# Kernel optimization log

Hardware: AMD Instinct MI355X
Metric: run time of the kernel (lower is better)

The kernel has to match this reference:

```python
import jax, jax.numpy as jnp
import numpy as np

NEG = -1e9  # matches torch masked_fill value (additive, not -inf)

def setup_inputs() -> dict:
    key = jax.random.key(0)
    k1, k2, k3, k4 = jax.random.split(key, 4)
    B, H, S, D = 8, 16, 1024, 64
    q = jax.random.normal(k1, (B, H, S, D), dtype=jnp.float32)
    k = jax.random.normal(k2, (B, H, S, D), dtype=jnp.float32)
    v = jax.random.normal(k3, (B, H, S, D), dtype=jnp.float32)
    event_length = jax.random.randint(k4, (B,), 0, S, dtype=jnp.int32)
    return {"q": q, "k": k, "v": v, "event_length": event_length}

def reference(q, k, v, event_length):
    B, H, S, D = q.shape
    scale = 1.0 / jnp.sqrt(jnp.asarray(D, dtype=q.dtype))
    idx = jnp.arange(S)
    # valid[b, i] = i < event_length[b]
    valid = idx[None, :] < event_length[:, None]            # [B, S]
    # additive mask: 0 where (row valid AND col valid), else -1e9
    pair = valid[:, :, None] & valid[:, None, :]            # [B, S, S]
    attn_mask = jnp.where(pair, 0.0, NEG).astype(q.dtype)[:, None, :, :]  # [B,1,S,S]
    scores = jnp.einsum('bhqd,bhkd->bhqk', q, k) * scale + attn_mask
    probs = jax.nn.softmax(scores, axis=-1)
    out = jnp.einsum('bhqk,bhkd->bhqd', probs, v)
    return out
```

## Files before the change

### kernel.cpp

```cpp
#include <hip/hip_runtime.h>


#define Sdim 1024
#define Ddim 64
#define PITCH 72

typedef float f32x4 __attribute__((ext_vector_type(4)));
typedef _Float16 f16x8 __attribute__((ext_vector_type(8)));
typedef _Float16 f16x4 __attribute__((ext_vector_type(4)));
typedef unsigned short u16x8 __attribute__((ext_vector_type(8)));
typedef unsigned int u32x2 __attribute__((ext_vector_type(2)));

union FragU { u16x8 u; f16x8 h; };
union Frag4 { u32x2 u; f16x4 h; };

__device__ __forceinline__ unsigned pk2(float a, float b) {
  auto h = __builtin_amdgcn_cvt_pkrtz(a, b);
  return __builtin_bit_cast(unsigned, h);
}

__device__ __forceinline__ float fexp2(float x) {
  float r;
  asm("v_exp_f32 %0, %1" : "=v"(r) : "v"(x));
  return r;
}

__global__ __launch_bounds__(256, 3)
void attn_fwd(const float* __restrict__ Q, const float* __restrict__ K,
              const float* __restrict__ V, const int* __restrict__ EL,
              float* __restrict__ Out, unsigned* __restrict__ queues) {
  __shared__ unsigned short lds_all[2 * 64 * PITCH];
  __shared__ int s_item;
  unsigned short* k_lds = lds_all;
  unsigned short* v_lds = lds_all + 64 * PITCH;

  const int tid   = threadIdx.x;
  const int homeq = blockIdx.x & 7;
  unsigned* ctr = &queues[homeq * 32];

  const int w    = tid >> 6;
  const int lane = tid & 63;
  const int r    = lane & 15;
  const int hi   = lane >> 4;
  const int r3   = r >> 3;
  const int sr   = tid >> 4;
  const int sc   = tid & 15;
  const int vskew = ((sc >> 1) & 7) * 8;

  for (;;) {
    __syncthreads();
    if (tid == 0) s_item = (int)atomicAdd(ctr, 1u);
    __syncthreads();
    const int g = s_item;
    if (g >= 128) break;

    const int pan = g >> 3;
    const int qt  = g & 7;
    const int bh  = pan * 8 + homeq;
    const int L   = EL[bh >> 4];

    const size_t base = (size_t)bh * Sdim * Ddim;
    const float* Qb = Q + base;
    const float* Kb = K + base;
    const float* Vb = V + base;
    float* ob = Out + base;

    const int q0blk = qt * 128;

    if (q0blk >= L) {
      float* red = (float*)lds_all;
      const int sc4 = sc * 4;
      const float* vp = Vb + (size_t)sr * Ddim + sc4;
      float4 acc = {0.f, 0.f, 0.f, 0.f};
#pragma unroll 8
      for (int i = 0; i < 64; ++i) {
        float4 a = *(const float4*)(vp + (size_t)i * 16 * Ddim);
        acc.x += a.x; acc.y += a.y; acc.z += a.z; acc.w += a.w;
      }
      *(float4*)&red[sr * 68 + sc4] = acc;
      __syncthreads();
      if (tid < 16) {
        float4 s = {0.f, 0.f, 0.f, 0.f};
#pragma unroll
        for (int i = 0; i < 16; ++i) {
          float4 a = *(const float4*)&red[i * 68 + tid * 4];
          s.x += a.x; s.y += a.y; s.z += a.z; s.w += a.w;
        }
        const float inv = 1.0f / 1024.0f;
        s.x *= inv; s.y *= inv; s.z *= inv; s.w *= inv;
        *(float4*)&red[16 * 68 + tid * 4] = s;
      }
      __syncthreads();
      const float4 cm = *(const float4*)&red[16 * 68 + sc4];
#pragma unroll
      for (int pp = 0; pp < 8; ++pp) {
        int row = q0blk + pp * 16 + sr;
        *(float4*)&ob[(size_t)row * Ddim + sc4] = cm;
      }
      continue;
    }

    const int q0w      = q0blk + w * 32;
    const bool wValid  = q0w < L;
    const bool wAllVal = (q0w + 32) <= L;
    const int kFull    = (L + 63) >> 6;
    const int ktB      = L >> 6;
    const bool straddle = (q0blk + 128) > L;

    const bool qv0 = (q0w + r) < L;
    const bool qv1 = (q0w + 16 + r) < L;

    const float SCL = 0.125f * 1.44269504088896340736f;
    f16x8 qf[2][2];
    if (wValid) {
#pragma unroll
      for (int qc = 0; qc < 2; ++qc)
#pragma unroll
        for (int kk = 0; kk < 2; ++kk) {
          const float* pq = Qb + (size_t)(q0w + qc * 16 + r) * Ddim + kk * 32 + hi * 8;
          float4 a = *(const float4*)pq;
          float4 cc = *(const float4*)(pq + 4);
          union { unsigned u[4]; f16x8 hh; } f;
          f.u[0] = pk2(a.x * SCL, a.y * SCL);   f.u[1] = pk2(a.z * SCL, a.w * SCL);
          f.u[2] = pk2(cc.x * SCL, cc.y * SCL); f.u[3] = pk2(cc.z * SCL, cc.w * SCL);
          qf[qc][kk] = f.hh;
        }
    }

    const f32x4 zero4 = {0.f, 0.f, 0.f, 0.f};
    f32x4 otacc[2][4];
#pragma unroll
    for (int qc = 0; qc < 2; ++qc)
#pragma unroll
      for (int dc = 0; dc < 4; ++dc) otacc[qc][dc] = zero4;

    float lpart[2] = {0.f, 0.f};

    const float* pK = Kb + (size_t)sr * Ddim + sc * 4;
    const float* pV = Vb + (size_t)(sr * 4) * Ddim + sc * 4;

    float4 kpre[4], vpre[4];
    auto LOADK = [&](int k0_) {
#pragma unroll
      for (int i = 0; i < 4; ++i)
        kpre[i] = *(const float4*)(pK + (size_t)(k0_ + 16 * i) * Ddim);
    };
    auto LOADV = [&](int k0_) {
#pragma unroll
      for (int jj = 0; jj < 4; ++jj)
        vpre[jj] = *(const float4*)(pV + (size_t)(k0_ + jj) * Ddim);
    };

    LOADK(0);
    LOADV(0);

    for (int kt = 0; kt < kFull; ++kt) {
      const int k0 = kt * 64;
      __syncthreads();

#pragma unroll
      for (int i = 0; i < 4; ++i) {
        u32x2 o;
        o[0] = pk2(kpre[i].x, kpre[i].y); o[1] = pk2(kpre[i].z, kpre[i].w);
        *(u32x2*)&k_lds[(16 * i + sr) * PITCH + sc * 4] = o;
      }
      {
        const int cp = (sr * 4 + vskew) & 63;
        u32x2 o;
        o[0] = pk2(vpre[0].x, vpre[1].x); o[1] = pk2(vpre[2].x, vpre[3].x);
        *(u32x2*)&v_lds[(sc * 4 + 0) * PITCH + cp] = o;
        o[0] = pk2(vpre[0].y, vpre[1].y); o[1] = pk2(vpre[2].y, vpre[3].y);
        *(u32x2*)&v_lds[(sc * 4 + 1) * PITCH + cp] = o;
        o[0] = pk2(vpre[0].z, vpre[1].z); o[1] = pk2(vpre[2].z, vpre[3].z);
        *(u32x2*)&v_lds[(sc * 4 + 2) * PITCH + cp] = o;
        o[0] = pk2(vpre[0].w, vpre[1].w); o[1] = pk2(vpre[2].w, vpre[3].w);
        *(u32x2*)&v_lds[(sc * 4 + 3) * PITCH + cp] = o;
      }
      __syncthreads();

      if (kt + 1 < kFull) { LOADK(k0 + 64); LOADV(k0 + 64); }

      if (wValid) {
        f32x4 sacc[2][4];
#pragma unroll
        for (int qc = 0; qc < 2; ++qc)
#pragma unroll
          for (int kc = 0; kc < 4; ++kc) sacc[qc][kc] = zero4;

        __builtin_amdgcn_s_setprio(1);
#pragma unroll
        for (int kc = 0; kc < 4; ++kc)
#pragma unroll
          for (int kk = 0; kk < 2; ++kk) {
            FragU kf;
            kf.u = *(const u16x8*)&k_lds[(kc * 16 + r) * PITCH + kk * 32 + hi * 8];
            sacc[0][kc] = __builtin_amdgcn_mfma_f32_16x16x32_f16(kf.h, qf[0][kk], sacc[0][kc], 0, 0, 0);
            sacc[1][kc] = __builtin_amdgcn_mfma_f32_16x16x32_f16(kf.h, qf[1][kk], sacc[1][kc], 0, 0, 0);
          }
        __builtin_amdgcn_s_setprio(0);

        const bool noMask = wAllVal && (kt != ktB);
        Frag4 pf[2][4];
#pragma unroll
        for (int qc = 0; qc < 2; ++qc) {
          const bool qv = qc ? qv1 : qv0;
          float ls = 0.f;
#pragma unroll
          for (int kc = 0; kc < 4; ++kc) {
            float pr[4];
#pragma unroll
            for (int rg = 0; rg < 4; ++rg) {
              float s = sacc[qc][kc][rg];
              if (!noMask) {
                int kg = k0 + kc * 16 + 4 * hi + rg;
                s = (qv && kg < L) ? s : -__builtin_inff();
              }
              pr[rg] = fexp2(s);
              ls += pr[rg];
            }
            pf[qc][kc].u[0] = pk2(pr[0], pr[1]);
            pf[qc][kc].u[1] = pk2(pr[2], pr[3]);
          }
          lpart[qc] += ls;
        }

        __builtin_amdgcn_s_setprio(1);
#pragma unroll
        for (int kc = 0; kc < 4; ++kc)
#pragma unroll
          for (int dc = 0; dc < 4; ++dc) {
            const int col = (kc * 16 + 4 * hi + (((2 * dc + r3) & 7) << 3)) & 63;
            Frag4 vf;
            vf.u = *(const u32x2*)&v_lds[(dc * 16 + r) * PITCH + col];
            otacc[0][dc] = __builtin_amdgcn_mfma_f32_16x16x16f16(vf.h, pf[0][kc].h, otacc[0][dc], 0, 0, 0);
            otacc[1][dc] = __builtin_amdgcn_mfma_f32_16x16x16f16(vf.h, pf[1][kc].h, otacc[1][dc], 0, 0, 0);
          }
        __builtin_amdgcn_s_setprio(0);
      }
    }

    __syncthreads();
    float* scr = (float*)lds_all + w * (16 * 68);
#pragma unroll
    for (int qc = 0; qc < 2; ++qc) {
      float l = lpart[qc];
      l += __shfl_xor(l, 16, 64);
      l += __shfl_xor(l, 32, 64);
      const float inv = 1.0f / l;
      if (wValid) {
#pragma unroll
        for (int dc = 0; dc < 4; ++dc)
#pragma unroll
          for (int rg = 0; rg < 4; ++rg)
            scr[r * 68 + dc * 16 + 4 * hi + rg] = otacc[qc][dc][rg] * inv;
      }
      asm volatile("s_waitcnt lgkmcnt(0)" ::: "memory");
      __builtin_amdgcn_sched_barrier(0);
      if (wValid) {
        const int rowq = lane >> 2, cs = lane & 3;
        const int q = q0w + qc * 16 + rowq;
        if (q < L) {
#pragma unroll
          for (int i = 0; i < 4; ++i) {
            float4 vv = *(const float4*)&scr[rowq * 68 + cs * 16 + i * 4];
            *(float4*)&ob[(size_t)q * Ddim + cs * 16 + i * 4] = vv;
          }
        }
      }
      asm volatile("s_waitcnt lgkmcnt(0)" ::: "memory");
      __builtin_amdgcn_sched_barrier(0);
    }

    if (straddle) {
      __syncthreads();
      float* red = (float*)lds_all;
      const int sc4 = sc * 4;
      const float* vp = Vb + (size_t)sr * Ddim + sc4;
      float4 acc = {0.f, 0.f, 0.f, 0.f};
#pragma unroll 8
      for (int i = 0; i < 64; ++i) {
        float4 a = *(const float4*)(vp + (size_t)i * 16 * Ddim);
        acc.x += a.x; acc.y += a.y; acc.z += a.z; acc.w += a.w;
      }
      *(float4*)&red[sr * 68 + sc4] = acc;
      __syncthreads();
      if (tid < 16) {
        float4 s = {0.f, 0.f, 0.f, 0.f};
#pragma unroll
        for (int i = 0; i < 16; ++i) {
          float4 a = *(const float4*)&red[i * 68 + tid * 4];
          s.x += a.x; s.y += a.y; s.z += a.z; s.w += a.w;
        }
        const float inv = 1.0f / 1024.0f;
        s.x *= inv; s.y *= inv; s.z *= inv; s.w *= inv;
        *(float4*)&red[16 * 68 + tid * 4] = s;
      }
      __syncthreads();
      const float4 cm = *(const float4*)&red[16 * 68 + sc4];
#pragma unroll
      for (int pp = 0; pp < 8; ++pp) {
        int row = q0blk + pp * 16 + sr;
        if (row >= L)
          *(float4*)&ob[(size_t)row * Ddim + sc4] = cm;
      }
    }
  }
}

extern "C" void kernel_launch(void* const* d_in, const int* in_sizes, int n_in,
                              void* d_out, int out_size, void* d_ws, size_t ws_size,
                              hipStream_t stream) {
  const float* q  = (const float*)d_in[0];
  const float* k  = (const float*)d_in[1];
  const float* v  = (const float*)d_in[2];
  const int*   el = (const int*)d_in[3];
  float* out = (float*)d_out;
  hipMemsetAsync(d_ws, 0, 1024, stream);
  dim3 grid(1024);
  dim3 block(256);
  hipLaunchKernelGGL(attn_fwd, grid, block, 0, stream, q, k, v, el, out,
                     (unsigned*)d_ws);
}
```

Measured before the change: 49.31 us.

## Load K fragments directly from global memory and double-buffer V in LDS

K is no longer staged through LDS. Each wave now loads its K MFMA fragments straight from global memory, converts them to fp16 in registers, and feeds them to the QK^T MFMAs. V moves to a two-slot LDS buffer indexed by kt parity, which removes one of the two __syncthreads per key tile. The intended gain is fewer LDS round trips and barriers, paid for with redundant global K reads across the 4 waves and global latency exposed directly in front of the MFMAs. A dead store to kf0 is left in.

```diff
diff --git a/kernel.cpp b/kernel.cpp
--- a/kernel.cpp
+++ b/kernel.cpp
@@ -29,10 +29,8 @@
 void attn_fwd(const float* __restrict__ Q, const float* __restrict__ K,
               const float* __restrict__ V, const int* __restrict__ EL,
               float* __restrict__ Out, unsigned* __restrict__ queues) {
-  __shared__ unsigned short lds_all[2 * 64 * PITCH];
+  __shared__ unsigned short vbuf[2][64 * PITCH];
   __shared__ int s_item;
-  unsigned short* k_lds = lds_all;
-  unsigned short* v_lds = lds_all + 64 * PITCH;
 
   const int tid   = threadIdx.x;
   const int homeq = blockIdx.x & 7;
@@ -68,7 +66,7 @@
     const int q0blk = qt * 128;
 
     if (q0blk >= L) {
-      float* red = (float*)lds_all;
+      float* red = (float*)&vbuf[0][0];
       const int sc4 = sc * 4;
       const float* vp = Vb + (size_t)sr * Ddim + sc4;
       float4 acc = {0.f, 0.f, 0.f, 0.f};
@@ -136,34 +134,22 @@
 
     float lpart[2] = {0.f, 0.f};
 
-    const float* pK = Kb + (size_t)sr * Ddim + sc * 4;
-    const float* pV = Vb + (size_t)(sr * 4) * Ddim + sc * 4;
-
-    float4 kpre[4], vpre[4];
-    auto LOADK = [&](int k0_) {
-#pragma unroll
-      for (int i = 0; i < 4; ++i)
-        kpre[i] = *(const float4*)(pK + (size_t)(k0_ + 16 * i) * Ddim);
-    };
+    const float* pKd = Kb + (size_t)r * Ddim + hi * 8;
+    const float* pV  = Vb + (size_t)(sr * 4) * Ddim + sc * 4;
+
+    float4 vpre[4];
     auto LOADV = [&](int k0_) {
 #pragma unroll
       for (int jj = 0; jj < 4; ++jj)
         vpre[jj] = *(const float4*)(pV + (size_t)(k0_ + jj) * Ddim);
     };
 
-    LOADK(0);
     LOADV(0);
 
     for (int kt = 0; kt < kFull; ++kt) {
       const int k0 = kt * 64;
-      __syncthreads();
-
-#pragma unroll
-      for (int i = 0; i < 4; ++i) {
-        u32x2 o;
-        o[0] = pk2(kpre[i].x, kpre[i].y); o[1] = pk2(kpre[i].z, kpre[i].w);
-        *(u32x2*)&k_lds[(16 * i + sr) * PITCH + sc * 4] = o;
-      }
+      unsigned short* v_lds = &vbuf[kt & 1][0];
+
       {
         const int cp = (sr * 4 + vskew) & 63;
         u32x2 o;
@@ -176,9 +162,9 @@
         o[0] = pk2(vpre[0].w, vpre[1].w); o[1] = pk2(vpre[2].w, vpre[3].w);
         *(u32x2*)&v_lds[(sc * 4 + 3) * PITCH + cp] = o;
       }
-      __syncthreads();
-
-      if (kt + 1 < kFull) { LOADK(k0 + 64); LOADV(k0 + 64); }
+      if (kt + 1 < kFull) LOADV(k0 + 64);
+
+      __syncthreads();
 
       if (wValid) {
         f32x4 sacc[2][4];
@@ -189,14 +175,24 @@
 
         __builtin_amdgcn_s_setprio(1);
 #pragma unroll
-        for (int kc = 0; kc < 4; ++kc)
-#pragma unroll
-          for (int kk = 0; kk < 2; ++kk) {
-            FragU kf;
-            kf.u = *(const u16x8*)&k_lds[(kc * 16 + r) * PITCH + kk * 32 + hi * 8];
-            sacc[0][kc] = __builtin_amdgcn_mfma_f32_16x16x32_f16(kf.h, qf[0][kk], sacc[0][kc], 0, 0, 0);
-            sacc[1][kc] = __builtin_amdgcn_mfma_f32_16x16x32_f16(kf.h, qf[1][kk], sacc[1][kc], 0, 0, 0);
-          }
+        for (int kc = 0; kc < 4; ++kc) {
+          const float* kp = pKd + (size_t)(k0 + kc * 16) * Ddim;
+          float4 a0 = *(const float4*)(kp);
+          float4 a1 = *(const float4*)(kp + 4);
+          float4 b0 = *(const float4*)(kp + 32);
+          float4 b1 = *(const float4*)(kp + 36);
+          FragU kf0, kf1;
+          kf0.u[0] = (unsigned short)0;
+          union { unsigned u[4]; f16x8 hh; } f0, f1;
+          f0.u[0] = pk2(a0.x, a0.y); f0.u[1] = pk2(a0.z, a0.w);
+          f0.u[2] = pk2(a1.x, a1.y); f0.u[3] = pk2(a1.z, a1.w);
+          f1.u[0] = pk2(b0.x, b0.y); f1.u[1] = pk2(b0.z, b0.w);
+          f1.u[2] = pk2(b1.x, b1.y); f1.u[3] = pk2(b1.z, b1.w);
+          sacc[0][kc] = __builtin_amdgcn_mfma_f32_16x16x32_f16(f0.hh, qf[0][0], sacc[0][kc], 0, 0, 0);
+          sacc[1][kc] = __builtin_amdgcn_mfma_f32_16x16x32_f16(f0.hh, qf[1][0], sacc[1][kc], 0, 0, 0);
+          sacc[0][kc] = __builtin_amdgcn_mfma_f32_16x16x32_f16(f1.hh, qf[0][1], sacc[0][kc], 0, 0, 0);
+          sacc[1][kc] = __builtin_amdgcn_mfma_f32_16x16x32_f16(f1.hh, qf[1][1], sacc[1][kc], 0, 0, 0);
+        }
         __builtin_amdgcn_s_setprio(0);
 
         const bool noMask = wAllVal && (kt != ktB);
@@ -240,7 +236,7 @@
     }
 
     __syncthreads();
-    float* scr = (float*)lds_all + w * (16 * 68);
+    float* scr = (float*)&vbuf[0][0] + w * (16 * 68);
 #pragma unroll
     for (int qc = 0; qc < 2; ++qc) {
       float l = lpart[qc];
@@ -273,7 +269,7 @@
 
     if (straddle) {
       __syncthreads();
-      float* red = (float*)lds_all;
+      float* red = (float*)&vbuf[0][0];
       const int sc4 = sc * 4;
       const float* vp = Vb + (size_t)sr * Ddim + sc4;
       float4 acc = {0.f, 0.f, 0.f, 0.f};
```

Result: slower. 80.75 us (+63.8%).
